# Kernel tuning notes

Hardware: AMD Instinct MI355X
Metric: run time of the kernel (lower is better)

Reference implementation:

```python
import jax, jax.numpy as jnp
import numpy as np

T = 8192      # sequence length (scan steps)
D_IN = 1024   # input feature dim
H = 1024      # d_model (hidden size)


def setup_inputs() -> dict:
    key = jax.random.key(0)
    k1, k2, k3, k4 = jax.random.split(key, 4)
    inputs = jax.random.normal(k1, (T, D_IN), dtype=jnp.float32)
    terminations = jax.random.randint(k2, (T,), 0, 2) > 0  # bool [T]
    last_state = jnp.zeros((H,), dtype=jnp.float32)
    # GRUCell params (flax layout: input kernel with bias for all 3 gates;
    # recurrent kernel, bias only on the candidate 'n' gate).
    # Gate order within the 3H axis: [r, z, n].
    Wi = jax.random.normal(k3, (D_IN, 3 * H), dtype=jnp.float32) / np.sqrt(D_IN)
    bi = jnp.zeros((3 * H,), dtype=jnp.float32)
    Wh = jax.random.normal(k4, (H, 3 * H), dtype=jnp.float32) / np.sqrt(H)
    bhn = jnp.zeros((H,), dtype=jnp.float32)
    return {"inputs": inputs, "terminations": terminations, "last_state": last_state,
            "Wi": Wi, "bi": bi, "Wh": Wh, "bhn": bhn}


def reference(inputs, terminations, last_state, Wi, bi, Wh, bhn):
    # Precompute all input-side gate preactivations in one big GEMM: [T, 3H]
    gi_all = inputs @ Wi + bi

    def step(h, xs):
        gi, term = xs
        # reset_on_terminate: zero the carry when the episode terminated
        h = jnp.where(term, jnp.zeros_like(h), h)
        gh = h @ Wh                      # [3H], recurrent preactivations
        gi_r, gi_z, gi_n = jnp.split(gi, 3)
        gh_r, gh_z, gh_n = jnp.split(gh, 3)
        r = jax.nn.sigmoid(gi_r + gh_r)
        z = jax.nn.sigmoid(gi_z + gh_z)
        n = jnp.tanh(gi_n + r * (gh_n + bhn))
        h_new = (1.0 - z) * n + z * h    # flax GRUCell update
        # GRUout emits (new_c, (new_c, new_h)); flax GRUCell returns new_h twice
        return h_new, (h_new, h_new)

    _, (new_states, y_t) = jax.lax.scan(step, last_state, (gi_all, terminations))
    return (y_t, new_states)  # each [T, H]
```

## Files before the change

kernel.cpp:

```cpp
#include <hip/hip_runtime.h>
#include <stdint.h>

#define T_LEN 8192
#define DIN   1024
#define HD    1024
#define TH    3072
#define NB    16
#define SKINNY_MAX 160

typedef __attribute__((ext_vector_type(8))) short bf16x8;
typedef __attribute__((ext_vector_type(4))) float f32x4;

__device__ __forceinline__ unsigned short f2bf(float x) {
    union { float f; unsigned u; } v; v.f = x;
    unsigned r = v.u + 0x7FFFu + ((v.u >> 16) & 1u);
    return (unsigned short)(r >> 16);
}

__device__ __forceinline__ float bf2f(unsigned short x) {
    union { unsigned u; float f; } v; v.u = ((unsigned)x) << 16;
    return v.f;
}

__device__ __forceinline__ void gld16(const void* g, void* l) {
    __builtin_amdgcn_global_load_lds(
        (const __attribute__((address_space(1))) unsigned int*)(uintptr_t)g,
        (__attribute__((address_space(3))) unsigned int*)(uintptr_t)l,
        16, 0, 0);
}

__device__ __forceinline__ float sigm(float x) { return 1.f / (1.f + __expf(-x)); }
__device__ __forceinline__ float tanh_fast(float x) { return 1.f - 2.f / (1.f + __expf(2.f * x)); }

__global__ void cast_x(const float* __restrict__ X, unsigned short* __restrict__ Xb) {
    int idx = (blockIdx.x * 256 + threadIdx.x) * 4;
    float4 v = *(const float4*)(X + idx);
    ushort4 o; o.x = f2bf(v.x); o.y = f2bf(v.y); o.z = f2bf(v.z); o.w = f2bf(v.w);
    *(ushort4*)(Xb + idx) = o;
}

__global__ void transpose_cast(const float* __restrict__ Wi, const float* __restrict__ Wh,
                               unsigned short* __restrict__ WiT, unsigned short* __restrict__ WhT) {
    const float* src = blockIdx.z ? Wh : Wi;
    unsigned short* dst = blockIdx.z ? WhT : WiT;
    int n0 = blockIdx.x * 64, k0 = blockIdx.y * 64;
    __shared__ unsigned short tile[64][65];
    int tid = threadIdx.x;
    for (int p = 0; p < 16; p++) {
        int idx = tid + p * 256;
        int kl = idx >> 6, nl = idx & 63;
        tile[kl][nl] = f2bf(src[(size_t)(k0 + kl) * TH + n0 + nl]);
    }
    __syncthreads();
    for (int p = 0; p < 16; p++) {
        int idx = tid + p * 256;
        int nl = idx >> 6, kl = idx & 63;
        dst[(size_t)(n0 + nl) * 1024 + k0 + kl] = tile[kl][nl];
    }
}

__global__ void meta_kernel(const int* __restrict__ term, const float* __restrict__ last_state,
                            int* __restrict__ pos_list, int* __restrict__ meta) {
    __shared__ int part[1024];
    __shared__ int cnt[NB];
    __shared__ int cur[NB];
    __shared__ int flag;
    int tid = threadIdx.x;
    if (tid < NB) cnt[tid] = 0;
    if (tid == 0) flag = 0;
    __syncthreads();
    int base = tid * 8;
    int mx = -1;
    for (int u = 0; u < 8; u++) {
        int t = base + u;
        int s = (t == 0 || term[t] != 0) ? t : -1;
        mx = s > mx ? s : mx;
    }
    part[tid] = mx;
    __syncthreads();
    for (int d = 1; d < 1024; d <<= 1) {
        int a = part[tid];
        int b = (tid >= d) ? part[tid - d] : -1;
        __syncthreads();
        part[tid] = a > b ? a : b;
        __syncthreads();
    }
    int run = (tid > 0) ? part[tid - 1] : -1;
    int kk[8];
    for (int u = 0; u < 8; u++) {
        int t = base + u;
        int s = (t == 0 || term[t] != 0) ? t : -1;
        run = s > run ? s : run;
        int ls = t - run;
        int k = ls < NB ? ls : NB - 1;
        kk[u] = k;
        atomicAdd(&cnt[k], 1);
    }
    if (last_state[tid] != 0.0f) atomicOr(&flag, 1);
    __syncthreads();
    if (tid == 0) {
        int off = 0;
        for (int k = 0; k < NB; k++) {
            meta[k] = cnt[k];
            meta[NB + k] = off;
            cur[k] = off;
            off += cnt[k];
        }
        meta[2 * NB] = flag;
        meta[48] = 0;
    }
    __syncthreads();
    for (int u = 0; u < 8; u++) {
        int idx = atomicAdd(&cur[kk[u]], 1);
        pos_list[idx] = base + u;
    }
}

__global__ __launch_bounds__(256) void gemm_gi(const unsigned short* __restrict__ Xb,
                                               const unsigned short* __restrict__ WiT,
                                               const float* __restrict__ bi,
                                               float* __restrict__ gi) {
    __shared__ unsigned short As[128 * 32];
    __shared__ unsigned short Bs[128 * 32];
    int tid = threadIdx.x;
    int m0 = blockIdx.y * 128, n0 = blockIdx.x * 128;
    int lane = tid & 63, wave = tid >> 6;
    int wm = wave & 1, wn = wave >> 1;
    int quad = lane >> 4, l16 = lane & 15;
    f32x4 acc[4][4] = {};
    for (int kb = 0; kb < 32; kb++) {
        int k0 = kb * 32;
        for (int p = 0; p < 2; p++) {
            int c = tid + p * 256;
            int row = c >> 2, cb = c & 3;
            gld16(Xb + (size_t)(m0 + row) * 1024 + k0 + cb * 8, As + c * 8);
            gld16(WiT + (size_t)(n0 + row) * 1024 + k0 + cb * 8, Bs + c * 8);
        }
        __syncthreads();
        bf16x8 af[4], bfr[4];
        for (int i = 0; i < 4; i++)
            af[i] = *(const bf16x8*)(As + (wm * 64 + i * 16 + l16) * 32 + quad * 8);
        for (int j = 0; j < 4; j++)
            bfr[j] = *(const bf16x8*)(Bs + (wn * 64 + j * 16 + l16) * 32 + quad * 8);
        for (int i = 0; i < 4; i++)
            for (int j = 0; j < 4; j++)
                acc[i][j] = __builtin_amdgcn_mfma_f32_16x16x32_bf16(af[i], bfr[j], acc[i][j], 0, 0, 0);
        __syncthreads();
    }
    for (int j = 0; j < 4; j++) {
        int col = n0 + wn * 64 + j * 16 + l16;
        float bv = bi[col];
        for (int i = 0; i < 4; i++) {
            int rbase = m0 + wm * 64 + i * 16 + quad * 4;
            for (int r = 0; r < 4; r++)
                gi[(size_t)(rbase + r) * TH + col] = acc[i][j][r] + bv;
        }
    }
}

__global__ void pass0_kernel(const float* __restrict__ gi, const float* __restrict__ bhn,
                             const float* __restrict__ last_state, const float* __restrict__ Wh,
                             const int* __restrict__ term, const int* __restrict__ pos_list,
                             const int* __restrict__ meta, float* __restrict__ out,
                             unsigned short* __restrict__ hb) {
    int S0 = meta[0];
    int b = blockIdx.x;
    if (b >= S0) return;
    int t = pos_list[meta[NB] + b];
    int tid = threadIdx.x;
    bool ls_path = (t == 0) && (term[0] == 0) && (meta[2 * NB] != 0);
    for (int u = 0; u < 4; u++) {
        int j = tid + u * 256;
        float gr = gi[(size_t)t * TH + j];
        float gz = gi[(size_t)t * TH + 1024 + j];
        float gn = gi[(size_t)t * TH + 2048 + j];
        float hp = 0.f, ghr = 0.f, ghz = 0.f, ghn = 0.f;
        if (ls_path) {
            hp = last_state[j];
            for (int k = 0; k < 1024; k++) {
                float hk = last_state[k];
                const float* w = Wh + (size_t)k * TH;
                ghr += hk * w[j]; ghz += hk * w[1024 + j]; ghn += hk * w[2048 + j];
            }
        }
        float r = sigm(gr + ghr);
        float z = sigm(gz + ghz);
        float n = tanh_fast(gn + r * (ghn + bhn[j]));
        float h = (1.f - z) * n + z * hp;
        out[(size_t)t * HD + j] = h;
        out[(size_t)(T_LEN + t) * HD + j] = h;
        hb[(size_t)t * HD + j] = f2bf(h);
    }
}

__global__ __launch_bounds__(256) void pass_gemm(const float* __restrict__ gi,
                                                 const float* __restrict__ bhn,
                                                 const unsigned short* __restrict__ WhT,
                                                 const unsigned short* __restrict__ hb,
                                                 float* __restrict__ out,
                                                 unsigned short* __restrict__ hbw,
                                                 const int* __restrict__ pos_list,
                                                 const int* __restrict__ meta, int k) {
    int S = meta[k];
    int off = meta[NB + k];
    int tid = threadIdx.x;
    int lane = tid & 63, wave = tid >> 6;
    int quad = lane >> 4, l16 = lane & 15;

    if (S <= SKINNY_MAX) {
        if (S == 0) return;
        int nrt = (S + 15) >> 4;
        int ntask = 64 * nrt;
        int gwave = ((blockIdx.y * 16 + blockIdx.x) << 2) + wave;
        int nw = gridDim.x * gridDim.y * 4;
        for (int task = gwave; task < ntask; task += nw) {
            int ct = task & 63;
            int rt = task >> 6;
            int j = ct * 16 + l16;
            int ra = rt * 16 + l16;
            ra = ra < S ? ra : S - 1;
            int t_a = pos_list[off + ra];
            const unsigned short* ap = hb + (size_t)(t_a - 1) * HD + quad * 8;
            const unsigned short* bp = WhT + (size_t)j * 1024 + quad * 8;
            f32x4 acc[3] = {};
            #pragma unroll
            for (int ks = 0; ks < 32; ks++) {
                bf16x8 a  = *(const bf16x8*)(ap + ks * 32);
                bf16x8 b0 = *(const bf16x8*)(bp + ks * 32);
                bf16x8 b1 = *(const bf16x8*)(bp + 1048576 + ks * 32);
                bf16x8 b2 = *(const bf16x8*)(bp + 2097152 + ks * 32);
                acc[0] = __builtin_amdgcn_mfma_f32_16x16x32_bf16(a, b0, acc[0], 0, 0, 0);
                acc[1] = __builtin_amdgcn_mfma_f32_16x16x32_bf16(a, b1, acc[1], 0, 0, 0);
                acc[2] = __builtin_amdgcn_mfma_f32_16x16x32_bf16(a, b2, acc[2], 0, 0, 0);
            }
            #pragma unroll
            for (int r = 0; r < 4; r++) {
                int rr = rt * 16 + quad * 4 + r;
                if (rr >= S) continue;
                int t = pos_list[off + rr];
                const float* girow = gi + (size_t)t * TH;
                float hp = out[(size_t)(t - 1) * HD + j];
                float rgt = sigm(girow[j] + acc[0][r]);
                float zgt = sigm(girow[1024 + j] + acc[1][r]);
                float ngt = tanh_fast(girow[2048 + j] + rgt * (acc[2][r] + bhn[j]));
                float hv = (1.f - zgt) * ngt + zgt * hp;
                out[(size_t)t * HD + j] = hv;
                out[(size_t)(T_LEN + t) * HD + j] = hv;
                hbw[(size_t)t * HD + j] = f2bf(hv);
            }
        }
        return;
    }

    int r0 = blockIdx.y * 64;
    if (r0 >= S) return;
    int j0 = blockIdx.x * 64;
    __shared__ unsigned short As[4 * 64 * 32];
    __shared__ unsigned short Bs[4 * 192 * 32];
    int wm = wave & 1, wn = wave >> 1;

    int arow = tid >> 2, sub = tid & 3;
    bool av = (r0 + arow) < S;
    int t_a = av ? pos_list[off + r0 + arow] : 1;
    const unsigned short* hsrc = hb + (size_t)(t_a - 1) * HD + sub * 8;

    f32x4 acc[2][6] = {};
    for (int kb = 0; kb < 8; kb++) {
        int k0 = kb * 128;
        for (int ks = 0; ks < 4; ks++) {
            int kk0 = k0 + ks * 32;
            for (int p = 0; p < 3; p++) {
                int c = tid + p * 256;
                int row = c >> 2, q = c & 3;
                int g = row >> 6, jj = row & 63;
                gld16(WhT + (size_t)(g * 1024 + j0 + jj) * 1024 + kk0 + q * 8,
                      Bs + ks * 6144 + c * 8);
            }
            gld16(hsrc + kk0, As + ks * 2048 + tid * 8);
        }
        __syncthreads();
        for (int ks = 0; ks < 4; ks++) {
            bf16x8 af[2];
            for (int i = 0; i < 2; i++)
                af[i] = *(const bf16x8*)(As + ks * 2048 + (wm * 32 + i * 16 + l16) * 32 + quad * 8);
            for (int n = 0; n < 6; n++) {
                int g = n >> 1, jh = n & 1;
                bf16x8 bv = *(const bf16x8*)(Bs + ks * 6144 + (g * 64 + wn * 32 + jh * 16 + l16) * 32 + quad * 8);
                for (int i = 0; i < 2; i++)
                    acc[i][n] = __builtin_amdgcn_mfma_f32_16x16x32_bf16(af[i], bv, acc[i][n], 0, 0, 0);
            }
        }
        __syncthreads();
    }
    for (int i = 0; i < 2; i++) {
        for (int r = 0; r < 4; r++) {
            int rr = r0 + wm * 32 + i * 16 + quad * 4 + r;
            if (rr >= S) continue;
            int t = pos_list[off + rr];
            const float* girow = gi + (size_t)t * TH;
            const float* hprow = out + (size_t)(t - 1) * HD;
            float* o1 = out + (size_t)t * HD;
            float* o2 = out + (size_t)(T_LEN + t) * HD;
            unsigned short* hbrow = hbw + (size_t)t * HD;
            for (int jh = 0; jh < 2; jh++) {
                int j = j0 + wn * 32 + jh * 16 + l16;
                float ghr = acc[i][0 + jh][r];
                float ghz = acc[i][2 + jh][r];
                float ghn = acc[i][4 + jh][r];
                float rg = sigm(girow[j] + ghr);
                float zg = sigm(girow[1024 + j] + ghz);
                float ng = tanh_fast(girow[2048 + j] + rg * (ghn + bhn[j]));
                float h = (1.f - zg) * ng + zg * hprow[j];
                o1[j] = h;
                o2[j] = h;
                hbrow[j] = f2bf(h);
            }
        }
    }
}

__global__ __launch_bounds__(256) void tail_pll(const float* __restrict__ gi,
                                                const float* __restrict__ bhn,
                                                const unsigned short* __restrict__ WhT,
                                                const int* __restrict__ pos_list,
                                                const int* __restrict__ meta,
                                                int* __restrict__ sync,
                                                float* __restrict__ out) {
    int S = meta[NB - 1];
    if (S == 0) return;
    __shared__ int pos[T_LEN];
    __shared__ float hsh[HD];
    __shared__ float dots[192];
    int off = meta[NB + NB - 1];
    int tid = threadIdx.x;
    int j0 = blockIdx.x * 64;
    for (int i = tid; i < S; i += 256) pos[i] = pos_list[off + i];
    __syncthreads();
    if (tid == 0) {
        for (int i = 1; i < S; i++) {
            int v = pos[i], j = i - 1;
            while (j >= 0 && pos[j] > v) { pos[j + 1] = pos[j]; j--; }
            pos[j + 1] = v;
        }
    }
    __syncthreads();
    for (int s = 0; s < S; s++) {
        int t = pos[s];
        for (int u = 0; u < 4; u++)
            hsh[tid + u * 256] = out[(size_t)(t - 1) * HD + tid + u * 256];
        __syncthreads();
        if (tid < 192) {
            int g = tid >> 6, jj = tid & 63;
            int col = g * 1024 + j0 + jj;
            const unsigned short* wrow = WhT + (size_t)col * 1024;
            float acc = 0.f;
            for (int kk = 0; kk < 1024; kk += 8) {
                bf16x8 wv = *(const bf16x8*)(wrow + kk);
                f32x4 h0 = *(const f32x4*)(hsh + kk);
                f32x4 h1 = *(const f32x4*)(hsh + kk + 4);
                acc += h0[0] * bf2f((unsigned short)wv[0]) + h0[1] * bf2f((unsigned short)wv[1])
                     + h0[2] * bf2f((unsigned short)wv[2]) + h0[3] * bf2f((unsigned short)wv[3])
                     + h1[0] * bf2f((unsigned short)wv[4]) + h1[1] * bf2f((unsigned short)wv[5])
                     + h1[2] * bf2f((unsigned short)wv[6]) + h1[3] * bf2f((unsigned short)wv[7]);
            }
            dots[tid] = acc;
        }
        __syncthreads();
        if (tid < 64) {
            int j = j0 + tid;
            float rg = sigm(gi[(size_t)t * TH + j] + dots[tid]);
            float zg = sigm(gi[(size_t)t * TH + 1024 + j] + dots[64 + tid]);
            float ng = tanh_fast(gi[(size_t)t * TH + 2048 + j] + rg * (dots[128 + tid] + bhn[j]));
            float hv = (1.f - zg) * ng + zg * hsh[j];
            out[(size_t)t * HD + j] = hv;
            out[(size_t)(T_LEN + t) * HD + j] = hv;
        }
        __threadfence();
        __syncthreads();
        if (tid == 0) {
            atomicAdd(sync, 1);
            int tgt = 16 * (s + 1);
            while (atomicAdd(sync, 0) < tgt)
                __builtin_amdgcn_s_sleep(8);
        }
        __syncthreads();
        __threadfence();
    }
}

extern "C" void kernel_launch(void* const* d_in, const int* in_sizes, int n_in,
                              void* d_out, int out_size, void* d_ws, size_t ws_size,
                              hipStream_t stream) {
    const float* X          = (const float*)d_in[0];
    const int*   term       = (const int*)d_in[1];
    const float* last_state = (const float*)d_in[2];
    const float* Wi         = (const float*)d_in[3];
    const float* bi         = (const float*)d_in[4];
    const float* Wh         = (const float*)d_in[5];
    const float* bhn        = (const float*)d_in[6];
    float* out = (float*)d_out;

    char* ws = (char*)d_ws;
    float*          gi       = (float*)ws;
    unsigned short* Xb       = (unsigned short*)(ws + 100663296);
    unsigned short* hb       = Xb;
    unsigned short* WiT      = (unsigned short*)(ws + 117440512);
    unsigned short* WhT      = (unsigned short*)(ws + 123731968);
    int*            pos_list = (int*)(ws + 130023424);
    int*            meta     = (int*)(ws + 130056192);
    int*            syncv    = meta + 48;

    cast_x<<<dim3(8192), dim3(256), 0, stream>>>(X, Xb);
    transpose_cast<<<dim3(48, 16, 2), dim3(256), 0, stream>>>(Wi, Wh, WiT, WhT);
    meta_kernel<<<dim3(1), dim3(1024), 0, stream>>>(term, last_state, pos_list, meta);
    gemm_gi<<<dim3(24, 64), dim3(256), 0, stream>>>(Xb, WiT, bi, gi);
    pass0_kernel<<<dim3(8192), dim3(256), 0, stream>>>(gi, bhn, last_state, Wh, term, pos_list, meta, out, hb);
    for (int k = 1; k < NB - 1; k++) {
        int rows_max = T_LEN / (k + 1);
        int gy = (rows_max + 63) / 64;
        pass_gemm<<<dim3(16, gy), dim3(256), 0, stream>>>(gi, bhn, WhT, hb, out, hb, pos_list, meta, k);
    }
    tail_pll<<<dim3(16), dim3(256), 0, stream>>>(gi, bhn, WhT, pos_list, meta, syncv, out);
}
```

Measured before the change: 430.8 us.

## Fuse later skinny recurrence passes into one persistent kernel with grid barrier

```diff
diff --git a/kernel.cpp b/kernel.cpp
--- a/kernel.cpp
+++ b/kernel.cpp
@@ -7,6 +7,7 @@
 #define TH    3072
 #define NB    16
 #define SKINNY_MAX 160
+#define KSPLIT 5
 
 typedef __attribute__((ext_vector_type(8))) short bf16x8;
 typedef __attribute__((ext_vector_type(4))) float f32x4;
@@ -108,6 +109,7 @@
         }
         meta[2 * NB] = flag;
         meta[48] = 0;
+        meta[49] = 0;
     }
     __syncthreads();
     for (int u = 0; u < 8; u++) {
@@ -123,7 +125,9 @@
     __shared__ unsigned short As[128 * 32];
     __shared__ unsigned short Bs[128 * 32];
     int tid = threadIdx.x;
-    int m0 = blockIdx.y * 128, n0 = blockIdx.x * 128;
+    int phys = blockIdx.y * gridDim.x + blockIdx.x;
+    int logi = (phys & 7) * 192 + (phys >> 3);
+    int m0 = (logi / 24) * 128, n0 = (logi % 24) * 128;
     int lane = tid & 63, wave = tid >> 6;
     int wm = wave & 1, wn = wave >> 1;
     int quad = lane >> 4, l16 = lane & 15;
@@ -319,6 +323,75 @@
     }
 }
 
+__global__ __launch_bounds__(256) void skinny_all(const float* __restrict__ gi,
+                                                  const float* __restrict__ bhn,
+                                                  const unsigned short* __restrict__ WhT,
+                                                  unsigned short* __restrict__ hb,
+                                                  float* __restrict__ out,
+                                                  const int* __restrict__ pos_list,
+                                                  const int* __restrict__ meta,
+                                                  int* __restrict__ syncc) {
+    int tid = threadIdx.x;
+    int lane = tid & 63, wave = tid >> 6;
+    int quad = lane >> 4, l16 = lane & 15;
+    int gwave = (blockIdx.x << 2) + wave;
+    int gen = 0;
+    for (int k = KSPLIT; k <= NB - 2; k++) {
+        int S = meta[k];
+        if (S == 0) break;
+        int off = meta[NB + k];
+        int nrt = (S + 15) >> 4;
+        int ntask = 64 * nrt;
+        for (int task = gwave; task < ntask; task += 512) {
+            int ct = task & 63;
+            int rt = task >> 6;
+            int j = ct * 16 + l16;
+            int ra = rt * 16 + l16;
+            ra = ra < S ? ra : S - 1;
+            int t_a = pos_list[off + ra];
+            const unsigned short* ap = hb + (size_t)(t_a - 1) * HD + quad * 8;
+            const unsigned short* bp = WhT + (size_t)j * 1024 + quad * 8;
+            f32x4 acc[3] = {};
+            #pragma unroll
+            for (int ks = 0; ks < 32; ks++) {
+                bf16x8 a  = *(const bf16x8*)(ap + ks * 32);
+                bf16x8 b0 = *(const bf16x8*)(bp + ks * 32);
+                bf16x8 b1 = *(const bf16x8*)(bp + 1048576 + ks * 32);
+                bf16x8 b2 = *(const bf16x8*)(bp + 2097152 + ks * 32);
+                acc[0] = __builtin_amdgcn_mfma_f32_16x16x32_bf16(a, b0, acc[0], 0, 0, 0);
+                acc[1] = __builtin_amdgcn_mfma_f32_16x16x32_bf16(a, b1, acc[1], 0, 0, 0);
+                acc[2] = __builtin_amdgcn_mfma_f32_16x16x32_bf16(a, b2, acc[2], 0, 0, 0);
+            }
+            #pragma unroll
+            for (int r = 0; r < 4; r++) {
+                int rr = rt * 16 + quad * 4 + r;
+                if (rr >= S) continue;
+                int t = pos_list[off + rr];
+                const float* girow = gi + (size_t)t * TH;
+                float hp = out[(size_t)(t - 1) * HD + j];
+                float rgt = sigm(girow[j] + acc[0][r]);
+                float zgt = sigm(girow[1024 + j] + acc[1][r]);
+                float ngt = tanh_fast(girow[2048 + j] + rgt * (acc[2][r] + bhn[j]));
+                float hv = (1.f - zgt) * ngt + zgt * hp;
+                out[(size_t)t * HD + j] = hv;
+                out[(size_t)(T_LEN + t) * HD + j] = hv;
+                hb[(size_t)t * HD + j] = f2bf(hv);
+            }
+        }
+        if (k == NB - 2 || meta[k + 1] == 0) break;
+        gen++;
+        __syncthreads();
+        __threadfence();
+        if (tid == 0) {
+            atomicAdd(syncc, 1);
+            while (atomicAdd(syncc, 0) < 128 * gen)
+                __builtin_amdgcn_s_sleep(4);
+        }
+        __syncthreads();
+        __threadfence();
+    }
+}
+
 __global__ __launch_bounds__(256) void tail_pll(const float* __restrict__ gi,
                                                 const float* __restrict__ bhn,
                                                 const unsigned short* __restrict__ WhT,
@@ -408,17 +481,19 @@
     unsigned short* WhT      = (unsigned short*)(ws + 123731968);
     int*            pos_list = (int*)(ws + 130023424);
     int*            meta     = (int*)(ws + 130056192);
-    int*            syncv    = meta + 48;
+    int*            sync_t   = meta + 48;
+    int*            sync_s   = meta + 49;
 
     cast_x<<<dim3(8192), dim3(256), 0, stream>>>(X, Xb);
     transpose_cast<<<dim3(48, 16, 2), dim3(256), 0, stream>>>(Wi, Wh, WiT, WhT);
     meta_kernel<<<dim3(1), dim3(1024), 0, stream>>>(term, last_state, pos_list, meta);
     gemm_gi<<<dim3(24, 64), dim3(256), 0, stream>>>(Xb, WiT, bi, gi);
     pass0_kernel<<<dim3(8192), dim3(256), 0, stream>>>(gi, bhn, last_state, Wh, term, pos_list, meta, out, hb);
-    for (int k = 1; k < NB - 1; k++) {
+    for (int k = 1; k < KSPLIT; k++) {
         int rows_max = T_LEN / (k + 1);
         int gy = (rows_max + 63) / 64;
         pass_gemm<<<dim3(16, gy), dim3(256), 0, stream>>>(gi, bhn, WhT, hb, out, hb, pos_list, meta, k);
     }
-    tail_pll<<<dim3(16), dim3(256), 0, stream>>>(gi, bhn, WhT, pos_list, meta, syncv, out);
-}
+    skinny_all<<<dim3(128), dim3(256), 0, stream>>>(gi, bhn, WhT, hb, out, pos_list, meta, sync_s);
+    tail_pll<<<dim3(16), dim3(256), 0, stream>>>(gi, bhn, WhT, pos_list, meta, sync_t, out);
+}
```

Result: slower. 507.5 us (+17.8%).
